# Performance work log

Hardware: AMD Instinct MI355X
Metric: run time of the kernel (lower is better)

## Reference

```python
import jax, jax.numpy as jnp
import numpy as np

VERY_NEGATIVE_NUMBER = -1e29

B, TC, TQ, D = 32, 2048, 256, 256


def setup_inputs() -> dict:
    key = jax.random.key(0)
    k1, k2, k3, k4 = jax.random.split(key, 4)
    context_repr = jax.random.normal(k1, (B, TC, D), dtype=jnp.float32)
    question_repr = jax.random.normal(k2, (B, TQ, D), dtype=jnp.float32)
    # lengths in [1, maxlen] so no row is fully masked
    context_len = jax.random.randint(k3, (B,), 1, TC + 1, dtype=jnp.int32)
    question_len = jax.random.randint(k4, (B,), 1, TQ + 1, dtype=jnp.int32)
    return {
        "context_repr": context_repr,
        "question_repr": question_repr,
        "context_len": context_len,
        "question_len": question_len,
    }


def reference(context_repr, question_repr, context_len, question_len):
    dtype = context_repr.dtype
    Tc = context_repr.shape[1]
    Tq = question_repr.shape[1]
    # similarity: dot product over feature dim -> [B, Tc, Tq]
    sim_mat = jnp.einsum("bcd,bqd->bcq", context_repr, question_repr)
    # sequence masks
    cmask = (jnp.arange(Tc)[None, :] < context_len[:, None]).astype(dtype)  # [B,Tc]
    qmask = (jnp.arange(Tq)[None, :] < question_len[:, None]).astype(dtype)  # [B,Tq]
    mask = cmask[:, :, None] * qmask[:, None, :]  # [B,Tc,Tq]
    sim_mat = sim_mat + (1.0 - mask) * VERY_NEGATIVE_NUMBER
    # context-to-query attention
    c2q_prob = jax.nn.softmax(sim_mat, axis=-1)  # [B,Tc,Tq]
    context2query_attention = jnp.einsum("bcq,bqd->bcd", c2q_prob, question_repr)
    # query-to-context attention: row-wise max then softmax over context positions
    q2c_prob = jax.nn.softmax(jnp.max(sim_mat, axis=-1), axis=-1)  # [B,Tc]
    q2c = jnp.einsum("bc,bcd->bd", q2c_prob, context_repr)  # [B,D]
    query2context_attention = jnp.broadcast_to(
        q2c[:, None, :], context2query_attention.shape
    )
    return (context2query_attention, query2context_attention)
```

## Files before the change

### kernel.cpp

```cpp
#include <hip/hip_runtime.h>
#include <hip/hip_fp16.h>

#define DEVI __device__ __forceinline__

typedef float f32x4 __attribute__((ext_vector_type(4)));
typedef float float4v __attribute__((ext_vector_type(4)));
typedef _Float16 f16x8 __attribute__((ext_vector_type(8)));
typedef unsigned short us8 __attribute__((ext_vector_type(8)));

constexpr int NB = 32, TC = 2048, TQ = 256, DD = 256;
constexpr int CR = 64;
constexpr float VNEG = -1e29f;

DEVI unsigned short f2h(float f) {
  _Float16 h = (_Float16)f;
  return __builtin_bit_cast(unsigned short, h);
}
DEVI float h2f(unsigned short u) {
  return (float)__builtin_bit_cast(_Float16, u);
}

DEVI int swz(int row, int cb) { return cb ^ (((row ^ (cb >> 7)) & 7) << 4); }

DEVI f32x4 mfmah(us8 a, us8 b, f32x4 c) {
  return __builtin_amdgcn_mfma_f32_16x16x32_f16(
      __builtin_bit_cast(f16x8, a), __builtin_bit_cast(f16x8, b), c, 0, 0, 0);
}

__global__ void P0(const float* __restrict__ Qg, unsigned short* __restrict__ Qh,
                   unsigned short* __restrict__ QT)
{
  __shared__ unsigned short t[64][72];
  const int bid = blockIdx.x, tid = threadIdx.x;
  const int b = bid >> 4;
  const int q0 = ((bid >> 2) & 3) * 64, d0 = (bid & 3) * 64;
  {
    const int qr = tid >> 2, dp = (tid & 3) * 16;
    const float* src = Qg + ((size_t)b * TQ + q0 + qr) * DD + d0 + dp;
    unsigned short* dst = Qh + ((size_t)b * TQ + q0 + qr) * DD + d0 + dp;
    us8 o0, o1;
#pragma unroll
    for (int i = 0; i < 4; ++i) {
      float4v v = *(const float4v*)(src + i * 4);
#pragma unroll
      for (int j = 0; j < 4; ++j) {
        const unsigned short h = f2h(v[j]);
        t[qr][dp + i * 4 + j] = h;
        if (i < 2) o0[i * 4 + j] = h; else o1[(i - 2) * 4 + j] = h;
      }
    }
    *(us8*)dst = o0;
    *(us8*)(dst + 8) = o1;
  }
  __syncthreads();
  {
    const int dr = tid >> 2, qp = (tid & 3) * 16;
    us8 a, c;
#pragma unroll
    for (int i = 0; i < 8; ++i) a[i] = t[qp + i][dr];
#pragma unroll
    for (int i = 0; i < 8; ++i) c[i] = t[qp + 8 + i][dr];
    unsigned short* dst = QT + ((size_t)b * DD + d0 + dr) * TQ + q0 + qp;
    *(us8*)dst = a;
    *(us8*)(dst + 8) = c;
  }
}

__global__ __launch_bounds__(512, 4)
void kA(const float* __restrict__ Cg, const unsigned short* __restrict__ Qh,
        const unsigned short* __restrict__ QT,
        const int* __restrict__ clenp, const int* __restrict__ qlenp,
        float* __restrict__ out1, float* __restrict__ pnum,
        float* __restrict__ ptM, float* __restrict__ ptD)
{
  __shared__ __align__(16) char lds[32768];
  __shared__ float redM[512];
  __shared__ float redS[512];
  __shared__ float wred[64];
  __shared__ float wexp[64];
  __shared__ float sinv[64];
  char* const bufC = lds;
  char* const bufP = lds;

  const int bid = blockIdx.x;
  const int b = bid & 31;
  const int tile = bid >> 5;
  const int c0 = tile * CR;
  const int tid = threadIdx.x;
  const int l = tid & 63, wid = tid >> 6;
  const int g = l >> 4, lm = l & 15;
  const int clen = clenp[b], qlen = qlenp[b];

  const float* Cb = Cg + (size_t)(b * TC + c0) * DD;
  const unsigned short* Qhb = Qh + (size_t)b * TQ * DD;
  const unsigned short* QTb = QT + (size_t)b * DD * TQ;

  us8 bq[16];
#pragma unroll
  for (int kk = 0; kk < 8; ++kk)
#pragma unroll
    for (int nt = 0; nt < 2; ++nt)
      bq[kk * 2 + nt] = *(const us8*)(Qhb + (size_t)(wid * 32 + nt * 16 + lm) * DD +
                                      kk * 32 + g * 8);

  {
    const int r = tid >> 3;
    const int d0 = (tid & 7) * 32;
    const float* src = Cb + (size_t)r * DD + d0;
#pragma unroll
    for (int i = 0; i < 4; ++i) {
      us8 h;
#pragma unroll
      for (int k = 0; k < 8; k += 4) {
        float4v v = *(const float4v*)(src + i * 8 + k);
#pragma unroll
        for (int j = 0; j < 4; ++j) h[k + j] = f2h(v[j]);
      }
      *(us8*)(bufC + r * 512 + swz(r, (d0 + i * 8) * 2)) = h;
    }
  }
  __syncthreads();

  f32x4 acc[4][2];
#pragma unroll
  for (int mt = 0; mt < 4; ++mt)
#pragma unroll
    for (int nt = 0; nt < 2; ++nt) acc[mt][nt] = (f32x4)0.0f;

#pragma unroll
  for (int kk = 0; kk < 8; ++kk) {
    us8 ah[4];
#pragma unroll
    for (int mt = 0; mt < 4; ++mt) {
      const int row = mt * 16 + lm;
      ah[mt] = *(const us8*)(bufC + row * 512 + swz(row, kk * 64 + g * 16));
    }
#pragma unroll
    for (int mt = 0; mt < 4; ++mt)
#pragma unroll
      for (int nt = 0; nt < 2; ++nt)
        acc[mt][nt] = mfmah(ah[mt], bq[kk * 2 + nt], acc[mt][nt]);
  }

#pragma unroll
  for (int nt = 0; nt < 2; ++nt) {
    const int q = wid * 32 + nt * 16 + lm;
    const bool qm = q >= qlen;
#pragma unroll
    for (int mt = 0; mt < 4; ++mt)
#pragma unroll
      for (int j = 0; j < 4; ++j) {
        const int c = c0 + mt * 16 + g * 4 + j;
        if (qm || c >= clen) acc[mt][nt][j] = VNEG;
      }
  }

#pragma unroll
  for (int mt = 0; mt < 4; ++mt)
#pragma unroll
    for (int j = 0; j < 4; ++j) {
      float m = fmaxf(acc[mt][0][j], acc[mt][1][j]);
      m = fmaxf(m, __shfl_xor(m, 1, 64));
      m = fmaxf(m, __shfl_xor(m, 2, 64));
      m = fmaxf(m, __shfl_xor(m, 4, 64));
      m = fmaxf(m, __shfl_xor(m, 8, 64));
      if (lm == 0) redM[wid * 64 + mt * 16 + g * 4 + j] = m;
    }
  __syncthreads();

  if (tid < 64) {
    float m = redM[tid];
#pragma unroll
    for (int w = 1; w < 8; ++w) m = fmaxf(m, redM[w * 64 + tid]);
    wred[tid] = m;
  }
  __syncthreads();

#pragma unroll
  for (int mt = 0; mt < 4; ++mt)
#pragma unroll
    for (int j = 0; j < 4; ++j) {
      const float m = wred[mt * 16 + g * 4 + j];
      float s = 0.f;
#pragma unroll
      for (int nt = 0; nt < 2; ++nt) {
        const float p = __expf(acc[mt][nt][j] - m);
        acc[mt][nt][j] = p;
        s += p;
      }
      s += __shfl_xor(s, 1, 64);
      s += __shfl_xor(s, 2, 64);
      s += __shfl_xor(s, 4, 64);
      s += __shfl_xor(s, 8, 64);
      if (lm == 0) redS[wid * 64 + mt * 16 + g * 4 + j] = s;
    }
  if (wid == 0) {
    float m = wred[l];
    m = fmaxf(m, __shfl_xor(m, 1, 64));  m = fmaxf(m, __shfl_xor(m, 2, 64));
    m = fmaxf(m, __shfl_xor(m, 4, 64));  m = fmaxf(m, __shfl_xor(m, 8, 64));
    m = fmaxf(m, __shfl_xor(m, 16, 64)); m = fmaxf(m, __shfl_xor(m, 32, 64));
    const float wv = __expf(wred[l] - m);
    wexp[l] = wv;
    float s = wv;
    s += __shfl_xor(s, 1, 64);  s += __shfl_xor(s, 2, 64);
    s += __shfl_xor(s, 4, 64);  s += __shfl_xor(s, 8, 64);
    s += __shfl_xor(s, 16, 64); s += __shfl_xor(s, 32, 64);
    if (l == 0) { ptD[b * 32 + tile] = s; ptM[b * 32 + tile] = m; }
  }
  __syncthreads();

  us8 qt[16];
#pragma unroll
  for (int kq = 0; kq < 8; ++kq)
#pragma unroll
    for (int dt = 0; dt < 2; ++dt)
      qt[kq * 2 + dt] = *(const us8*)(QTb + (size_t)(wid * 32 + dt * 16 + lm) * TQ +
                                      kq * 32 + g * 8);

  if (tid < 64) {
    float s = 0.f;
#pragma unroll
    for (int w = 0; w < 8; ++w) s += redS[w * 64 + tid];
    sinv[tid] = 1.0f / s;
  }

  {
    const int half = tid >> 8;
    const int d = tid & 255;
    float qacc = 0.f;
    const int d2 = d * 2;
#pragma unroll 8
    for (int r = half * 32; r < half * 32 + 32; ++r) {
      const float cv = h2f(*(const unsigned short*)(bufC + r * 512 + swz(r, d2)));
      qacc += wexp[r] * cv;
    }
    pnum[(((size_t)b * 32 + tile) * 2 + half) * DD + d] = qacc;
  }
  __syncthreads();

#pragma unroll
  for (int mt = 0; mt < 4; ++mt)
#pragma unroll
    for (int nt = 0; nt < 2; ++nt)
#pragma unroll
      for (int j = 0; j < 4; ++j) {
        const int row = mt * 16 + g * 4 + j;
        const int cb = (wid * 32 + nt * 16 + lm) * 2;
        *(unsigned short*)(bufP + row * 512 + swz(row, cb)) = f2h(acc[mt][nt][j]);
      }
  __syncthreads();

  f32x4 pacc[4][2];
#pragma unroll
  for (int mt = 0; mt < 4; ++mt)
#pragma unroll
    for (int dt = 0; dt < 2; ++dt) pacc[mt][dt] = (f32x4)0.0f;
#pragma unroll
  for (int kq = 0; kq < 8; ++kq) {
    us8 pa[4];
#pragma unroll
    for (int mt = 0; mt < 4; ++mt) {
      const int row = mt * 16 + lm;
      pa[mt] = *(const us8*)(bufP + row * 512 + swz(row, kq * 64 + g * 16));
    }
#pragma unroll
    for (int mt = 0; mt < 4; ++mt)
#pragma unroll
      for (int dt = 0; dt < 2; ++dt)
        pacc[mt][dt] = mfmah(pa[mt], qt[kq * 2 + dt], pacc[mt][dt]);
  }

#pragma unroll
  for (int mt = 0; mt < 4; ++mt)
#pragma unroll
    for (int j = 0; j < 4; ++j) {
      const int row = mt * 16 + g * 4 + j;
      const float inv = sinv[row];
      const size_t rowoff = (size_t)(b * TC + c0 + row) * DD;
#pragma unroll
      for (int dt = 0; dt < 2; ++dt)
        out1[rowoff + wid * 32 + dt * 16 + lm] = pacc[mt][dt][j] * inv;
    }
}

__global__ void kC(const float* __restrict__ pnum, const float* __restrict__ ptM,
                   const float* __restrict__ ptD, float* __restrict__ out2)
{
  const int b = blockIdx.x >> 4, seg = blockIdx.x & 15;
  const int d = threadIdx.x;
  __shared__ float sM[32], sD[32];
  if (d < 32) { sM[d] = ptM[b * 32 + d]; sD[d] = ptD[b * 32 + d]; }
  __syncthreads();
  float m = sM[0];
#pragma unroll
  for (int t = 1; t < 32; ++t) m = fmaxf(m, sM[t]);
  float den = 0.f, acc = 0.f;
#pragma unroll
  for (int t = 0; t < 32; ++t) {
    const float sc = __expf(sM[t] - m);
    den += sc * sD[t];
    const size_t base = (((size_t)b * 32 + t) * 2) * DD + d;
    acc += sc * (pnum[base] + pnum[base + DD]);
  }
  const float s = acc / den;
  float* dst = out2 + ((size_t)b * TC + seg * 128) * DD + d;
#pragma unroll 4
  for (int c = 0; c < 128; ++c) dst[(size_t)c * DD] = s;
}

extern "C" void kernel_launch(void* const* d_in, const int* in_sizes, int n_in,
                              void* d_out, int out_size, void* d_ws, size_t ws_size,
                              hipStream_t stream)
{
  const float* Cg = (const float*)d_in[0];
  const float* Qg = (const float*)d_in[1];
  const int* clen = (const int*)d_in[2];
  const int* qlen = (const int*)d_in[3];
  float* out1 = (float*)d_out;
  float* out2 = out1 + (size_t)NB * TC * DD;

  char* ws = (char*)d_ws;
  float* pnum = (float*)(ws);
  float* ptM  = (float*)(ws + 2097152);
  float* ptD  = (float*)(ws + 2101248);
  unsigned short* Qh = (unsigned short*)(ws + 2105344);
  unsigned short* QT = (unsigned short*)(ws + 2105344 + 4194304);

  P0 <<<dim3(512), dim3(256), 0, stream>>>(Qg, Qh, QT);
  kA <<<dim3(NB * (TC / CR)), dim3(512), 0, stream>>>(Cg, Qh, QT, clen, qlen,
                                                      out1, pnum, ptM, ptD);
  kC <<<dim3(NB * 16), dim3(256), 0, stream>>>(pnum, ptM, ptD, out2);
}
```

Measured before the change: 84.39 us.

## Process two context tiles per block and prefetch the second tile during softmax

New measurement: 113.5 us. 34.5% more time.

```diff
diff --git a/kernel.cpp b/kernel.cpp
--- a/kernel.cpp
+++ b/kernel.cpp
@@ -73,214 +73,247 @@
         float* __restrict__ out1, float* __restrict__ pnum,
         float* __restrict__ ptM, float* __restrict__ ptD)
 {
-  __shared__ __align__(16) char lds[32768];
+  __shared__ __align__(16) char lds0[32768];
+  __shared__ __align__(16) char lds1[32768];
   __shared__ float redM[512];
   __shared__ float redS[512];
   __shared__ float wred[64];
   __shared__ float wexp[64];
   __shared__ float sinv[64];
-  char* const bufC = lds;
-  char* const bufP = lds;
 
   const int bid = blockIdx.x;
   const int b = bid & 31;
-  const int tile = bid >> 5;
-  const int c0 = tile * CR;
+  const int slot = bid >> 5;
   const int tid = threadIdx.x;
   const int l = tid & 63, wid = tid >> 6;
   const int g = l >> 4, lm = l & 15;
   const int clen = clenp[b], qlen = qlenp[b];
 
-  const float* Cb = Cg + (size_t)(b * TC + c0) * DD;
   const unsigned short* Qhb = Qh + (size_t)b * TQ * DD;
   const unsigned short* QTb = QT + (size_t)b * DD * TQ;
 
-  us8 bq[16];
-#pragma unroll
-  for (int kk = 0; kk < 8; ++kk)
-#pragma unroll
-    for (int nt = 0; nt < 2; ++nt)
-      bq[kk * 2 + nt] = *(const us8*)(Qhb + (size_t)(wid * 32 + nt * 16 + lm) * DD +
-                                      kk * 32 + g * 8);
-
-  {
-    const int r = tid >> 3;
-    const int d0 = (tid & 7) * 32;
-    const float* src = Cb + (size_t)r * DD + d0;
-#pragma unroll
-    for (int i = 0; i < 4; ++i) {
-      us8 h;
-#pragma unroll
-      for (int k = 0; k < 8; k += 4) {
-        float4v v = *(const float4v*)(src + i * 8 + k);
-#pragma unroll
-        for (int j = 0; j < 4; ++j) h[k + j] = f2h(v[j]);
-      }
-      *(us8*)(bufC + r * 512 + swz(r, (d0 + i * 8) * 2)) = h;
-    }
-  }
-  __syncthreads();
-
-  f32x4 acc[4][2];
-#pragma unroll
-  for (int mt = 0; mt < 4; ++mt)
-#pragma unroll
-    for (int nt = 0; nt < 2; ++nt) acc[mt][nt] = (f32x4)0.0f;
-
-#pragma unroll
-  for (int kk = 0; kk < 8; ++kk) {
-    us8 ah[4];
-#pragma unroll
-    for (int mt = 0; mt < 4; ++mt) {
-      const int row = mt * 16 + lm;
-      ah[mt] = *(const us8*)(bufC + row * 512 + swz(row, kk * 64 + g * 16));
-    }
-#pragma unroll
-    for (int mt = 0; mt < 4; ++mt)
+  const int r_st = tid >> 3;
+  const int d_st = (tid & 7) * 32;
+
+#pragma unroll
+  for (int t = 0; t < 2; ++t) {
+    const int tile = slot * 2 + t;
+    const int c0 = tile * CR;
+    char* const bufC = t ? lds1 : lds0;
+
+    if (t == 1) asm volatile("" ::: "memory");
+
+    us8 bq[16];
+#pragma unroll
+    for (int kk = 0; kk < 8; ++kk)
 #pragma unroll
       for (int nt = 0; nt < 2; ++nt)
-        acc[mt][nt] = mfmah(ah[mt], bq[kk * 2 + nt], acc[mt][nt]);
-  }
-
-#pragma unroll
-  for (int nt = 0; nt < 2; ++nt) {
-    const int q = wid * 32 + nt * 16 + lm;
-    const bool qm = q >= qlen;
+        bq[kk * 2 + nt] = *(const us8*)(Qhb +
+            (size_t)(wid * 32 + nt * 16 + lm) * DD + kk * 32 + g * 8);
+
+    if (t == 0) {
+      const float* src = Cg + (size_t)(b * TC + c0 + r_st) * DD + d_st;
+#pragma unroll
+      for (int i = 0; i < 4; ++i) {
+        us8 h;
+#pragma unroll
+        for (int k = 0; k < 8; k += 4) {
+          float4v v = *(const float4v*)(src + i * 8 + k);
+#pragma unroll
+          for (int j = 0; j < 4; ++j) h[k + j] = f2h(v[j]);
+        }
+        *(us8*)(bufC + r_st * 512 + swz(r_st, (d_st + i * 8) * 2)) = h;
+      }
+      __syncthreads();
+    }
+
+    f32x4 acc[4][2];
+#pragma unroll
+    for (int mt = 0; mt < 4; ++mt)
+#pragma unroll
+      for (int nt = 0; nt < 2; ++nt) acc[mt][nt] = (f32x4)0.0f;
+
+#pragma unroll
+    for (int kk = 0; kk < 8; ++kk) {
+      us8 ah[4];
+#pragma unroll
+      for (int mt = 0; mt < 4; ++mt) {
+        const int row = mt * 16 + lm;
+        ah[mt] = *(const us8*)(bufC + row * 512 + swz(row, kk * 64 + g * 16));
+      }
+#pragma unroll
+      for (int mt = 0; mt < 4; ++mt)
+#pragma unroll
+        for (int nt = 0; nt < 2; ++nt)
+          acc[mt][nt] = mfmah(ah[mt], bq[kk * 2 + nt], acc[mt][nt]);
+    }
+
+#pragma unroll
+    for (int nt = 0; nt < 2; ++nt) {
+      const int q = wid * 32 + nt * 16 + lm;
+      const bool qm = q >= qlen;
+#pragma unroll
+      for (int mt = 0; mt < 4; ++mt)
+#pragma unroll
+        for (int j = 0; j < 4; ++j) {
+          const int c = c0 + mt * 16 + g * 4 + j;
+          if (qm || c >= clen) acc[mt][nt][j] = VNEG;
+        }
+    }
+
 #pragma unroll
     for (int mt = 0; mt < 4; ++mt)
 #pragma unroll
       for (int j = 0; j < 4; ++j) {
-        const int c = c0 + mt * 16 + g * 4 + j;
-        if (qm || c >= clen) acc[mt][nt][j] = VNEG;
-      }
-  }
-
-#pragma unroll
-  for (int mt = 0; mt < 4; ++mt)
-#pragma unroll
-    for (int j = 0; j < 4; ++j) {
-      float m = fmaxf(acc[mt][0][j], acc[mt][1][j]);
-      m = fmaxf(m, __shfl_xor(m, 1, 64));
-      m = fmaxf(m, __shfl_xor(m, 2, 64));
-      m = fmaxf(m, __shfl_xor(m, 4, 64));
-      m = fmaxf(m, __shfl_xor(m, 8, 64));
-      if (lm == 0) redM[wid * 64 + mt * 16 + g * 4 + j] = m;
-    }
-  __syncthreads();
-
-  if (tid < 64) {
-    float m = redM[tid];
-#pragma unroll
-    for (int w = 1; w < 8; ++w) m = fmaxf(m, redM[w * 64 + tid]);
-    wred[tid] = m;
-  }
-  __syncthreads();
-
-#pragma unroll
-  for (int mt = 0; mt < 4; ++mt)
-#pragma unroll
-    for (int j = 0; j < 4; ++j) {
-      const float m = wred[mt * 16 + g * 4 + j];
+        float m = fmaxf(acc[mt][0][j], acc[mt][1][j]);
+        m = fmaxf(m, __shfl_xor(m, 1, 64));
+        m = fmaxf(m, __shfl_xor(m, 2, 64));
+        m = fmaxf(m, __shfl_xor(m, 4, 64));
+        m = fmaxf(m, __shfl_xor(m, 8, 64));
+        if (lm == 0) redM[wid * 64 + mt * 16 + g * 4 + j] = m;
+      }
+    __syncthreads();
+
+    if (tid < 64) {
+      float m = redM[tid];
+#pragma unroll
+      for (int w = 1; w < 8; ++w) m = fmaxf(m, redM[w * 64 + tid]);
+      wred[tid] = m;
+    }
+    __syncthreads();
+
+    float4v cr[8];
+    if (t == 0) {
+      const float* src2 = Cg + (size_t)(b * TC + slot * 2 * CR + CR + r_st) * DD + d_st;
+#pragma unroll
+      for (int i = 0; i < 8; ++i) cr[i] = *(const float4v*)(src2 + i * 4);
+    }
+
+#pragma unroll
+    for (int mt = 0; mt < 4; ++mt)
+#pragma unroll
+      for (int j = 0; j < 4; ++j) {
+        const float m = wred[mt * 16 + g * 4 + j];
+        float s = 0.f;
+#pragma unroll
+        for (int nt = 0; nt < 2; ++nt) {
+          const float p = __expf(acc[mt][nt][j] - m);
+          acc[mt][nt][j] = p;
+          s += p;
+        }
+        s += __shfl_xor(s, 1, 64);
+        s += __shfl_xor(s, 2, 64);
+        s += __shfl_xor(s, 4, 64);
+        s += __shfl_xor(s, 8, 64);
+        if (lm == 0) redS[wid * 64 + mt * 16 + g * 4 + j] = s;
+      }
+    if (wid == 0) {
+      float m = wred[l];
+      m = fmaxf(m, __shfl_xor(m, 1, 64));  m = fmaxf(m, __shfl_xor(m, 2, 64));
+      m = fmaxf(m, __shfl_xor(m, 4, 64));  m = fmaxf(m, __shfl_xor(m, 8, 64));
+      m = fmaxf(m, __shfl_xor(m, 16, 64)); m = fmaxf(m, __shfl_xor(m, 32, 64));
+      const float wv = __expf(wred[l] - m);
+      wexp[l] = wv;
+      float s = wv;
+      s += __shfl_xor(s, 1, 64);  s += __shfl_xor(s, 2, 64);
+      s += __shfl_xor(s, 4, 64);  s += __shfl_xor(s, 8, 64);
+      s += __shfl_xor(s, 16, 64); s += __shfl_xor(s, 32, 64);
+      if (l == 0) { ptD[b * 32 + tile] = s; ptM[b * 32 + tile] = m; }
+    }
+    __syncthreads();
+
+    us8 qt[16];
+#pragma unroll
+    for (int kq = 0; kq < 4; ++kq)
+#pragma unroll
+      for (int dt = 0; dt < 2; ++dt)
+        qt[kq * 2 + dt] = *(const us8*)(QTb +
+            (size_t)(wid * 32 + dt * 16 + lm) * TQ + kq * 32 + g * 8);
+
+    if (tid < 64) {
       float s = 0.f;
 #pragma unroll
-      for (int nt = 0; nt < 2; ++nt) {
-        const float p = __expf(acc[mt][nt][j] - m);
-        acc[mt][nt][j] = p;
-        s += p;
-      }
-      s += __shfl_xor(s, 1, 64);
-      s += __shfl_xor(s, 2, 64);
-      s += __shfl_xor(s, 4, 64);
-      s += __shfl_xor(s, 8, 64);
-      if (lm == 0) redS[wid * 64 + mt * 16 + g * 4 + j] = s;
-    }
-  if (wid == 0) {
-    float m = wred[l];
-    m = fmaxf(m, __shfl_xor(m, 1, 64));  m = fmaxf(m, __shfl_xor(m, 2, 64));
-    m = fmaxf(m, __shfl_xor(m, 4, 64));  m = fmaxf(m, __shfl_xor(m, 8, 64));
-    m = fmaxf(m, __shfl_xor(m, 16, 64)); m = fmaxf(m, __shfl_xor(m, 32, 64));
-    const float wv = __expf(wred[l] - m);
-    wexp[l] = wv;
-    float s = wv;
-    s += __shfl_xor(s, 1, 64);  s += __shfl_xor(s, 2, 64);
-    s += __shfl_xor(s, 4, 64);  s += __shfl_xor(s, 8, 64);
-    s += __shfl_xor(s, 16, 64); s += __shfl_xor(s, 32, 64);
-    if (l == 0) { ptD[b * 32 + tile] = s; ptM[b * 32 + tile] = m; }
-  }
-  __syncthreads();
-
-  us8 qt[16];
-#pragma unroll
-  for (int kq = 0; kq < 8; ++kq)
-#pragma unroll
-    for (int dt = 0; dt < 2; ++dt)
-      qt[kq * 2 + dt] = *(const us8*)(QTb + (size_t)(wid * 32 + dt * 16 + lm) * TQ +
-                                      kq * 32 + g * 8);
-
-  if (tid < 64) {
-    float s = 0.f;
-#pragma unroll
-    for (int w = 0; w < 8; ++w) s += redS[w * 64 + tid];
-    sinv[tid] = 1.0f / s;
-  }
-
-  {
-    const int half = tid >> 8;
-    const int d = tid & 255;
-    float qacc = 0.f;
-    const int d2 = d * 2;
+      for (int w = 0; w < 8; ++w) s += redS[w * 64 + tid];
+      sinv[tid] = 1.0f / s;
+    }
+
+    {
+      const int half = tid >> 8;
+      const int d = tid & 255;
+      float qacc = 0.f;
+      const int d2 = d * 2;
 #pragma unroll 8
-    for (int r = half * 32; r < half * 32 + 32; ++r) {
-      const float cv = h2f(*(const unsigned short*)(bufC + r * 512 + swz(r, d2)));
-      qacc += wexp[r] * cv;
-    }
-    pnum[(((size_t)b * 32 + tile) * 2 + half) * DD + d] = qacc;
-  }
-  __syncthreads();
-
-#pragma unroll
-  for (int mt = 0; mt < 4; ++mt)
-#pragma unroll
-    for (int nt = 0; nt < 2; ++nt)
+      for (int r = half * 32; r < half * 32 + 32; ++r) {
+        const float cv = h2f(*(const unsigned short*)(bufC + r * 512 + swz(r, d2)));
+        qacc += wexp[r] * cv;
+      }
+      pnum[(((size_t)b * 32 + tile) * 2 + half) * DD + d] = qacc;
+    }
+
+    if (t == 0) {
+#pragma unroll
+      for (int i = 0; i < 4; ++i) {
+        us8 h;
+#pragma unroll
+        for (int j = 0; j < 4; ++j) h[j] = f2h(cr[2 * i][j]);
+#pragma unroll
+        for (int j = 0; j < 4; ++j) h[4 + j] = f2h(cr[2 * i + 1][j]);
+        *(us8*)(lds1 + r_st * 512 + swz(r_st, (d_st + i * 8) * 2)) = h;
+      }
+    }
+    __syncthreads();
+
+#pragma unroll
+    for (int mt = 0; mt < 4; ++mt)
+#pragma unroll
+      for (int nt = 0; nt < 2; ++nt)
+#pragma unroll
+        for (int j = 0; j < 4; ++j) {
+          const int row = mt * 16 + g * 4 + j;
+          const int cb = (wid * 32 + nt * 16 + lm) * 2;
+          *(unsigned short*)(bufC + row * 512 + swz(row, cb)) = f2h(acc[mt][nt][j]);
+        }
+    __syncthreads();
+
+#pragma unroll
+    for (int kq = 4; kq < 8; ++kq)
+#pragma unroll
+      for (int dt = 0; dt < 2; ++dt)
+        qt[kq * 2 + dt] = *(const us8*)(QTb +
+            (size_t)(wid * 32 + dt * 16 + lm) * TQ + kq * 32 + g * 8);
+
+    f32x4 pacc[4][2];
+#pragma unroll
+    for (int mt = 0; mt < 4; ++mt)
+#pragma unroll
+      for (int dt = 0; dt < 2; ++dt) pacc[mt][dt] = (f32x4)0.0f;
+#pragma unroll
+    for (int kq = 0; kq < 8; ++kq) {
+      us8 pa[4];
+#pragma unroll
+      for (int mt = 0; mt < 4; ++mt) {
+        const int row = mt * 16 + lm;
+        pa[mt] = *(const us8*)(bufC + row * 512 + swz(row, kq * 64 + g * 16));
+      }
+#pragma unroll
+      for (int mt = 0; mt < 4; ++mt)
+#pragma unroll
+        for (int dt = 0; dt < 2; ++dt)
+          pacc[mt][dt] = mfmah(pa[mt], qt[kq * 2 + dt], pacc[mt][dt]);
+    }
+
+#pragma unroll
+    for (int mt = 0; mt < 4; ++mt)
 #pragma unroll
       for (int j = 0; j < 4; ++j) {
         const int row = mt * 16 + g * 4 + j;
-        const int cb = (wid * 32 + nt * 16 + lm) * 2;
-        *(unsigned short*)(bufP + row * 512 + swz(row, cb)) = f2h(acc[mt][nt][j]);
-      }
-  __syncthreads();
-
-  f32x4 pacc[4][2];
-#pragma unroll
-  for (int mt = 0; mt < 4; ++mt)
-#pragma unroll
-    for (int dt = 0; dt < 2; ++dt) pacc[mt][dt] = (f32x4)0.0f;
-#pragma unroll
-  for (int kq = 0; kq < 8; ++kq) {
-    us8 pa[4];
-#pragma unroll
-    for (int mt = 0; mt < 4; ++mt) {
-      const int row = mt * 16 + lm;
-      pa[mt] = *(const us8*)(bufP + row * 512 + swz(row, kq * 64 + g * 16));
-    }
-#pragma unroll
-    for (int mt = 0; mt < 4; ++mt)
-#pragma unroll
-      for (int dt = 0; dt < 2; ++dt)
-        pacc[mt][dt] = mfmah(pa[mt], qt[kq * 2 + dt], pacc[mt][dt]);
+        const float inv = sinv[row];
+        const size_t rowoff = (size_t)(b * TC + c0 + row) * DD;
+#pragma unroll
+        for (int dt = 0; dt < 2; ++dt)
+          out1[rowoff + wid * 32 + dt * 16 + lm] = pacc[mt][dt][j] * inv;
+      }
   }
-
-#pragma unroll
-  for (int mt = 0; mt < 4; ++mt)
-#pragma unroll
-    for (int j = 0; j < 4; ++j) {
-      const int row = mt * 16 + g * 4 + j;
-      const float inv = sinv[row];
-      const size_t rowoff = (size_t)(b * TC + c0 + row) * DD;
-#pragma unroll
-      for (int dt = 0; dt < 2; ++dt)
-        out1[rowoff + wid * 32 + dt * 16 + lm] = pacc[mt][dt][j] * inv;
-    }
 }
 
 __global__ void kC(const float* __restrict__ pnum, const float* __restrict__ ptM,
@@ -327,7 +360,7 @@
   unsigned short* QT = (unsigned short*)(ws + 2105344 + 4194304);
 
   P0 <<<dim3(512), dim3(256), 0, stream>>>(Qg, Qh, QT);
-  kA <<<dim3(NB * (TC / CR)), dim3(512), 0, stream>>>(Cg, Qh, QT, clen, qlen,
-                                                      out1, pnum, ptM, ptD);
+  kA <<<dim3(512), dim3(512), 0, stream>>>(Cg, Qh, QT, clen, qlen,
+                                           out1, pnum, ptM, ptD);
   kC <<<dim3(NB * 16), dim3(256), 0, stream>>>(pnum, ptM, ptD, out2);
 }
```
